# Performance work log

Measured on AMD Instinct MI355X. Metric: run time of the kernel, lower is better.

Reference implementation:

```python
import jax, jax.numpy as jnp
import numpy as np

B, C, H, W = 2, 128, 64, 64
EPS = 1e-5


def setup_inputs() -> dict:
    key = jax.random.key(0)
    ks = jax.random.split(key, 8)
    sc = 1.0 / np.sqrt(C)
    inp = {
        "x": jax.random.normal(ks[0], (B, C, H, W, 2), jnp.float32),
        # naive complex BN affine params: per-channel, per-component (real/imag)
        "bn_w": jnp.ones((C, 2), jnp.float32),
        "bn_b": jnp.zeros((C, 2), jnp.float32),
        # complex 1x1 conv weights: (out_c, in_c, 2) -> [..,0]=W_real, [..,1]=W_imag
        "wq": jax.random.normal(ks[1], (C, C, 2), jnp.float32) * sc,
        "bq": jnp.zeros((C, 2), jnp.float32),
        "wk": jax.random.normal(ks[2], (C, C, 2), jnp.float32) * sc,
        "bk": jnp.zeros((C, 2), jnp.float32),
        "wv": jax.random.normal(ks[3], (C, C, 2), jnp.float32) * sc,
        "bv": jnp.zeros((C, 2), jnp.float32),
        "gamma": jnp.float32(0.05),
    }
    return inp


def _complex_bn(x, w, b):
    # naive complex BN: normalize real and imag independently per channel
    # x: (B,C,H,W,2); stats over (B,H,W) per (C, component)
    mean = x.mean(axis=(0, 2, 3), keepdims=True)
    var = x.var(axis=(0, 2, 3), keepdims=True)
    xn = (x - mean) * jax.lax.rsqrt(var + EPS)
    return xn * w[None, :, None, None, :] + b[None, :, None, None, :]


def _complex_conv1x1(x, w, b):
    # x: (B,C,H,W,2); w: (O,C,2); b: (O,2)
    xr, xi = x[..., 0], x[..., 1]
    wr, wi = w[..., 0], w[..., 1]
    yr = jnp.einsum('oc,bchw->bohw', wr, xr) - jnp.einsum('oc,bchw->bohw', wi, xi)
    yi = jnp.einsum('oc,bchw->bohw', wr, xi) + jnp.einsum('oc,bchw->bohw', wi, xr)
    yr = yr + b[:, 0][None, :, None, None]
    yi = yi + b[:, 1][None, :, None, None]
    return jnp.stack([yr, yi], axis=-1)


def _attention(x, wq, bq, wk, bk, wv, bv, gamma):
    scale = C ** (-0.5)
    N = H * W
    # q,k,v: (B,C,H,W,2) -> (B,C,N,2) -> (B,N,C,2)
    to_tokens = lambda t: t.reshape(B, C, N, 2).transpose(0, 2, 1, 3)
    q = to_tokens(_complex_conv1x1(x, wq, bq))
    k = to_tokens(_complex_conv1x1(x, wk, bk))
    v = to_tokens(_complex_conv1x1(x, wv, bv))

    qr, qi = q[..., 0], q[..., 1]          # (B,N,C)
    kr, ki = k[..., 0], -k[..., 1]         # conjugate of k
    # k_t = conj(k) with token/channel axes swapped -> (B,C,N)
    ktr = kr.transpose(0, 2, 1)
    kti = ki.transpose(0, 2, 1)

    # complex matmul q @ k_t -> only the real part is used downstream
    attn_real = jnp.einsum('bnc,bcm->bnm', qr, ktr) - jnp.einsum('bnc,bcm->bnm', qi, kti)
    attn_w = jax.nn.softmax(attn_real * scale, axis=-1)  # (B,N,N)
    # dropout = identity (eval mode)

    # attn is purely real -> complex matmul reduces to two real matmuls
    out_r = jnp.einsum('bnm,bmc->bnc', attn_w, v[..., 0])
    out_i = jnp.einsum('bnm,bmc->bnc', attn_w, v[..., 1])
    out = jnp.stack([out_r, out_i], axis=-1)              # (B,N,C,2)
    out = out.transpose(0, 2, 1, 3).reshape(B, C, H, W, 2)
    return x + gamma * out


def reference(x, bn_w, bn_b, wq, bq, wk, bk, wv, bv, gamma):
    xn = _complex_bn(x, bn_w, bn_b)
    return _attention(xn, wq, bq, wk, bk, wv, bv, gamma)
```

## Files before the change

### kernel.cpp

```cpp
#include <hip/hip_runtime.h>
#include <hip/hip_bf16.h>

typedef __bf16 bf16_t;
typedef __bf16 bf16x8 __attribute__((ext_vector_type(8)));
typedef float  f32x4  __attribute__((ext_vector_type(4)));

#define MFMA16(A,B,C) __builtin_amdgcn_mfma_f32_16x16x32_bf16((A),(B),(C),0,0,0)

constexpr int Bn = 2, Cc = 128, Hh = 64, Wd = 64;
constexpr int N  = Hh * Wd;
constexpr int T  = Bn * N;
constexpr int D  = 2 * Cc;
constexpr int NSP = 4;
constexpr float EPS = 1e-5f;
constexpr float SCL = 0.08838834764831845f * 1.4426950408889634f;

__device__ __forceinline__ int tfrag(int row, int ch) {
    return (((ch >> 5) * 4 + (row >> 4)) << 10) +
           ((((ch >> 3) & 3) * 16 + (row & 15)) << 4) + (ch & 7) * 2;
}
__device__ __forceinline__ int vfrag(int ch, int key) {
    return (((key >> 5) * 16 + (ch >> 4)) << 10) +
           ((((key >> 3) & 3) * 16 + (ch & 15)) << 4) + (key & 7) * 2;
}

__device__ __forceinline__ void gl16(const void* g, void* l) {
    __builtin_amdgcn_global_load_lds(
        (const __attribute__((address_space(1))) void*)g,
        (__attribute__((address_space(3))) void*)l, 16, 0, 0);
}

__global__ void k_pre(const float* __restrict__ x, float4* __restrict__ part,
                      const float* __restrict__ wq, const float* __restrict__ wk,
                      const float* __restrict__ wv, const float* __restrict__ bq,
                      const float* __restrict__ bk, const float* __restrict__ bv,
                      char* __restrict__ Wg, float* __restrict__ bt) {
    int tid = threadIdx.x;
    if (blockIdx.x < 512) {
        int bid = blockIdx.x;
        int q = bid >> 7, c = bid & 127;
        float sr = 0.f, si = 0.f, qr = 0.f, qi = 0.f;
        for (int b = 0; b < Bn; ++b) {
            const float2* p = (const float2*)x + (size_t)(b * Cc + c) * N + q * 1024;
            for (int i = tid; i < 1024; i += 256) {
                float2 v = p[i];
                sr += v.x; si += v.y; qr += v.x * v.x; qi += v.y * v.y;
            }
        }
        #pragma unroll
        for (int d = 32; d >= 1; d >>= 1) {
            sr += __shfl_xor(sr, d); si += __shfl_xor(si, d);
            qr += __shfl_xor(qr, d); qi += __shfl_xor(qi, d);
        }
        __shared__ float red[4][4];
        int w = tid >> 6;
        if ((tid & 63) == 0) { red[w][0] = sr; red[w][1] = si; red[w][2] = qr; red[w][3] = qi; }
        __syncthreads();
        if (tid == 0) {
            part[c * 4 + q] = make_float4(red[0][0] + red[1][0] + red[2][0] + red[3][0],
                                          red[0][1] + red[1][1] + red[2][1] + red[3][1],
                                          red[0][2] + red[1][2] + red[2][2] + red[3][2],
                                          red[0][3] + red[1][3] + red[2][3] + red[3][3]);
        }
    } else {
        int o = blockIdx.x - 512;
        int k = tid;
        int proj = o >> 8, oc = o & 255;
        const float* wsrc = proj == 0 ? wq : (proj == 1 ? wk : wv);
        const float* bsrc = proj == 0 ? bq : (proj == 1 ? bk : bv);
        int co = oc >> 7, oo = oc & 127;
        int c = k & 127, kc = k >> 7;
        float val;
        if (co == 0) val = (kc == 0) ? wsrc[(oo * 128 + c) * 2 + 0] : -wsrc[(oo * 128 + c) * 2 + 1];
        else         val = (kc == 0) ? wsrc[(oo * 128 + c) * 2 + 1] :  wsrc[(oo * 128 + c) * 2 + 0];
        int tile = o >> 6, row = o & 63;
        *(bf16_t*)(Wg + (size_t)tile * 32768 + tfrag(row, k)) = (bf16_t)val;
        if (k == 0) bt[o] = bsrc[oo * 2 + co];
    }
}

__global__ void k_norm(const float* __restrict__ x, const float4* __restrict__ part,
                       const float* __restrict__ bn_w, const float* __restrict__ bn_b,
                       char* __restrict__ XNg) {
    __shared__ float4 ssl[128];
    __shared__ __align__(16) char Tsh[32768];
    int blk = blockIdx.x;
    int b = blk >> 6, hw0 = (blk & 63) * 64;
    int tid = threadIdx.x;
    if (tid < 128) {
        float4 p0 = part[tid * 4 + 0], p1 = part[tid * 4 + 1];
        float4 p2 = part[tid * 4 + 2], p3 = part[tid * 4 + 3];
        float sr = p0.x + p1.x + p2.x + p3.x, si = p0.y + p1.y + p2.y + p3.y;
        float qr = p0.z + p1.z + p2.z + p3.z, qi = p0.w + p1.w + p2.w + p3.w;
        const float inv = 1.0f / (float)(Bn * N);
        float mr = sr * inv, mi = si * inv;
        float vr = qr * inv - mr * mr, vi = qi * inv - mi * mi;
        float scr = bn_w[tid * 2 + 0] * rsqrtf(vr + EPS);
        float sci = bn_w[tid * 2 + 1] * rsqrtf(vi + EPS);
        ssl[tid] = make_float4(scr, bn_b[tid * 2 + 0] - mr * scr,
                               sci, bn_b[tid * 2 + 1] - mi * sci);
    }
    __syncthreads();
    const float2* xin = (const float2*)x;
    #pragma unroll
    for (int it = 0; it < 32; ++it) {
        int idx = it * 256 + tid;
        int c = idx >> 6, hw = idx & 63;
        size_t gi = (size_t)(b * Cc + c) * N + hw0 + hw;
        float2 v = xin[gi];
        float4 s = ssl[c];
        *(bf16_t*)(Tsh + tfrag(hw, c))       = (bf16_t)(v.x * s.x + s.y);
        *(bf16_t*)(Tsh + tfrag(hw, c + 128)) = (bf16_t)(v.y * s.z + s.w);
    }
    __syncthreads();
    #pragma unroll
    for (int it = 0; it < 8; ++it) {
        int idx = it * 256 + tid;
        *(uint4*)(XNg + (size_t)blk * 32768 + idx * 16) = *(const uint4*)(Tsh + idx * 16);
    }
}

__global__ __launch_bounds__(256) void k_qkv(const char* __restrict__ XNg,
        const char* __restrict__ Wg, const float* __restrict__ bt,
        char* __restrict__ Qg, char* __restrict__ Kg, char* __restrict__ Vg) {
    __shared__ __align__(16) char Xsh[32768];
    __shared__ __align__(16) char Wsh[32768];
    int mx = blockIdx.x, ny = blockIdx.y;
    int tid = threadIdx.x;
    int w = tid >> 6, lane = tid & 63, n15 = lane & 15, quad = lane >> 4;
    const char* xs = XNg + (size_t)mx * 32768;
    const char* wsp = Wg + (size_t)ny * 32768;
    #pragma unroll
    for (int i = 0; i < 8; ++i) {
        int off = (w * 8 + i) * 1024 + lane * 16;
        gl16(xs + off, Xsh + off);
        gl16(wsp + off, Wsh + off);
    }
    __syncthreads();
    f32x4 acc[4] = {};
    #pragma unroll
    for (int ks = 0; ks < 8; ++ks) {
        bf16x8 a = *(const bf16x8*)(Xsh + (ks * 4 + w) * 1024 + lane * 16);
        #pragma unroll
        for (int t = 0; t < 4; ++t) {
            bf16x8 bw = *(const bf16x8*)(Wsh + (ks * 4 + t) * 1024 + lane * 16);
            acc[t] = MFMA16(a, bw, acc[t]);
        }
    }
    int proj = ny >> 2;
    int jb = (ny & 3) * 64;
    #pragma unroll
    for (int t = 0; t < 4; ++t) {
        int j = jb + t * 16 + n15;
        float bias = bt[ny * 64 + t * 16 + n15];
        #pragma unroll
        for (int r = 0; r < 4; ++r) {
            int tk = mx * 64 + w * 16 + quad * 4 + r;
            float v = acc[t][r] + bias;
            int bb = tk >> 12, n = tk & (N - 1);
            if (proj == 0) {
                *(bf16_t*)(Qg + (size_t)(tk >> 6) * 32768 + tfrag(tk & 63, j)) = (bf16_t)v;
            } else {
                size_t tb = (size_t)(bb * 64 + (n >> 6)) * 32768;
                if (proj == 1) *(bf16_t*)(Kg + tb + tfrag(n & 63, j)) = (bf16_t)v;
                else           *(bf16_t*)(Vg + tb + vfrag(j, n & 63)) = (bf16_t)v;
            }
        }
    }
}

__global__ __launch_bounds__(256, 2) void k_attn(const char* __restrict__ Qg,
        const char* __restrict__ Kg, const char* __restrict__ Vg,
        bf16_t* __restrict__ Opb, float* __restrict__ Lp) {
    __shared__ __align__(16) char Ksh[32768];
    __shared__ __align__(16) char Vsh[32768 + 1024];
    __shared__ __align__(16) char Psh[8192];
    int bid = blockIdx.x;
    int qt = bid & 63, sp = (bid >> 6) & 3, b = bid >> 8;
    int tid = threadIdx.x;
    int w = tid >> 6, lane = tid & 63, n15 = lane & 15, quad = lane >> 4;
    int r = w >> 1, h = w & 1;

    if (tid < 64) {
        uint4 ones; ones.x = ones.y = ones.z = ones.w = 0x3F803F80u;
        *(uint4*)(Vsh + 32768 + tid * 16) = ones;
    }

    bf16x8 qf[2][8];
    const char* qb = Qg + (size_t)(b * 64 + qt) * 32768;
    #pragma unroll
    for (int g = 0; g < 2; ++g)
        #pragma unroll
        for (int ks = 0; ks < 8; ++ks)
            qf[g][ks] = *(const bf16x8*)(qb + (ks * 4 + r * 2 + g) * 1024 + lane * 16);

    f32x4 o[2][8] = {};
    f32x4 l_[2] = {};

    for (int kt = 0; kt < 16; ++kt) {
        size_t tb = (size_t)(b * 64 + sp * 16 + kt) * 32768;
        __syncthreads();
        #pragma unroll
        for (int i = 0; i < 8; ++i) {
            int off = (w * 8 + i) * 1024 + lane * 16;
            gl16(Kg + tb + off, Ksh + off);
            gl16(Vg + tb + off, Vsh + off);
        }
        __syncthreads();

        f32x4 s[2][2] = {};
        #pragma unroll
        for (int ks = 0; ks < 8; ++ks) {
            #pragma unroll
            for (int c = 0; c < 2; ++c) {
                bf16x8 kf = *(const bf16x8*)(Ksh + (ks * 4 + h * 2 + c) * 1024 + lane * 16);
                s[0][c] = MFMA16(qf[0][ks], kf, s[0][c]);
                s[1][c] = MFMA16(qf[1][ks], kf, s[1][c]);
            }
        }
        #pragma unroll
        for (int g = 0; g < 2; ++g)
            #pragma unroll
            for (int c = 0; c < 2; ++c)
                #pragma unroll
                for (int ri = 0; ri < 4; ++ri) {
                    float p = __builtin_amdgcn_exp2f(s[g][c][ri] * SCL);
                    *(bf16_t*)(Psh + (h * 4 + r * 2 + g) * 1024 +
                               ((c * 2 + (n15 >> 3)) * 16 + quad * 4 + ri) * 16 +
                               (n15 & 7) * 2) = (bf16_t)p;
                }
        __syncthreads();
        #pragma unroll
        for (int k2 = 0; k2 < 2; ++k2) {
            bf16x8 pa0 = *(const bf16x8*)(Psh + (k2 * 4 + r * 2 + 0) * 1024 + lane * 16);
            bf16x8 pa1 = *(const bf16x8*)(Psh + (k2 * 4 + r * 2 + 1) * 1024 + lane * 16);
            bf16x8 onef = *(const bf16x8*)(Vsh + 32768 + lane * 16);
            l_[0] = MFMA16(pa0, onef, l_[0]);
            l_[1] = MFMA16(pa1, onef, l_[1]);
            #pragma unroll
            for (int ct = 0; ct < 8; ++ct) {
                bf16x8 vf = *(const bf16x8*)(Vsh + (k2 * 16 + h * 8 + ct) * 1024 + lane * 16);
                o[0][ct] = MFMA16(pa0, vf, o[0][ct]);
                o[1][ct] = MFMA16(pa1, vf, o[1][ct]);
            }
        }
    }
    int tok0 = b * N + qt * 64 + r * 32;
    #pragma unroll
    for (int g = 0; g < 2; ++g) {
        #pragma unroll
        for (int ct = 0; ct < 8; ++ct)
            #pragma unroll
            for (int ri = 0; ri < 4; ++ri)
                Opb[((size_t)sp * T + tok0 + g * 16 + quad * 4 + ri) * D +
                    h * 128 + ct * 16 + n15] = (bf16_t)o[g][ct][ri];
        if (h == 0 && n15 == 0) {
            #pragma unroll
            for (int ri = 0; ri < 4; ++ri)
                Lp[sp * T + tok0 + g * 16 + quad * 4 + ri] = l_[g][ri];
        }
    }
}

__global__ void k_comb(const bf16_t* __restrict__ Opb, const float* __restrict__ Lp,
                       const float4* __restrict__ part, const float* __restrict__ bn_w,
                       const float* __restrict__ bn_b, const float* __restrict__ x,
                       const float* __restrict__ gamma, float* __restrict__ out) {
    __shared__ float4 ssl[128];
    __shared__ float wts[32];
    __shared__ float Ot[256 * 33];
    int blk = blockIdx.x;
    int b = blk >> 7, hw0 = (blk & 127) * 32;
    int tok0 = b * N + hw0;
    int tid = threadIdx.x;
    if (tid < 128) {
        float4 p0 = part[tid * 4 + 0], p1 = part[tid * 4 + 1];
        float4 p2 = part[tid * 4 + 2], p3 = part[tid * 4 + 3];
        float sr = p0.x + p1.x + p2.x + p3.x, si = p0.y + p1.y + p2.y + p3.y;
        float qr = p0.z + p1.z + p2.z + p3.z, qi = p0.w + p1.w + p2.w + p3.w;
        const float inv = 1.0f / (float)(Bn * N);
        float mr = sr * inv, mi = si * inv;
        float vr = qr * inv - mr * mr, vi = qi * inv - mi * mi;
        float scr = bn_w[tid * 2 + 0] * rsqrtf(vr + EPS);
        float sci = bn_w[tid * 2 + 1] * rsqrtf(vi + EPS);
        ssl[tid] = make_float4(scr, bn_b[tid * 2 + 0] - mr * scr,
                               sci, bn_b[tid * 2 + 1] - mi * sci);
    }
    if (tid < 32) {
        float Z = 0.f;
        #pragma unroll
        for (int s = 0; s < NSP; ++s) Z += Lp[s * T + tok0 + tid];
        wts[tid] = gamma[0] / Z;
    }
    __syncthreads();
    #pragma unroll
    for (int i = 0; i < 4; ++i) {
        int idx = i * 256 + tid;
        int tk = idx >> 5, chunk = idx & 31;
        size_t base = (size_t)(tok0 + tk) * D + chunk * 8;
        float acc[8] = {};
        #pragma unroll
        for (int s = 0; s < NSP; ++s) {
            bf16x8 v = *(const bf16x8*)(Opb + (size_t)s * T * D + base);
            #pragma unroll
            for (int j = 0; j < 8; ++j) acc[j] += (float)v[j];
        }
        float ww = wts[tk];
        #pragma unroll
        for (int j = 0; j < 8; ++j) Ot[(chunk * 8 + j) * 33 + tk] = acc[j] * ww;
    }
    __syncthreads();
    const float2* xin = (const float2*)x;
    float2* xo = (float2*)out;
    #pragma unroll
    for (int i = 0; i < 16; ++i) {
        int linear = i * 256 + tid;
        int c = linear >> 5, hwo = linear & 31;
        size_t idx = (size_t)(b * Cc + c) * N + hw0 + hwo;
        float2 v = xin[idx];
        float4 s = ssl[c];
        float2 res;
        res.x = v.x * s.x + s.y + Ot[c * 33 + hwo];
        res.y = v.y * s.z + s.w + Ot[(128 + c) * 33 + hwo];
        xo[idx] = res;
    }
}

extern "C" void kernel_launch(void* const* d_in, const int* in_sizes, int n_in,
                              void* d_out, int out_size, void* d_ws, size_t ws_size,
                              hipStream_t stream) {
    const float* x    = (const float*)d_in[0];
    const float* bn_w = (const float*)d_in[1];
    const float* bn_b = (const float*)d_in[2];
    const float* wq   = (const float*)d_in[3];
    const float* bq   = (const float*)d_in[4];
    const float* wk   = (const float*)d_in[5];
    const float* bk   = (const float*)d_in[6];
    const float* wv   = (const float*)d_in[7];
    const float* bv   = (const float*)d_in[8];
    const float* gam  = (const float*)d_in[9];
    float* out = (float*)d_out;

    char* ws = (char*)d_ws;
    size_t off = 0;
    auto alloc = [&](size_t bytes) -> void* {
        void* p = ws + off;
        off += (bytes + 255) & ~(size_t)255;
        return p;
    };
    float4* part = (float4*)alloc(512 * sizeof(float4));
    char*   XNg  = (char*)alloc((size_t)128 * 32768);
    char*   Wg   = (char*)alloc((size_t)12 * 32768);
    float*  bt   = (float*)alloc(768 * 4);
    char*   Qg   = (char*)alloc((size_t)128 * 32768);
    char*   Kg   = (char*)alloc((size_t)128 * 32768);
    char*   Vg   = (char*)alloc((size_t)128 * 32768);
    bf16_t* Opb  = (bf16_t*)alloc((size_t)NSP * T * D * 2);
    float*  Lp   = (float*)alloc((size_t)NSP * T * 4);

    k_pre<<<1280, 256, 0, stream>>>(x, part, wq, wk, wv, bq, bk, bv, Wg, bt);
    k_norm<<<128, 256, 0, stream>>>(x, part, bn_w, bn_b, XNg);
    k_qkv<<<dim3(128, 12), 256, 0, stream>>>(XNg, Wg, bt, Qg, Kg, Vg);
    k_attn<<<512, 256, 0, stream>>>(Qg, Kg, Vg, Opb, Lp);
    k_comb<<<256, 256, 0, stream>>>(Opb, Lp, part, bn_w, bn_b, x, gam, out);
}
```

Measured before the change: 151.7 us.

## Double-buffer K tiles in half-size key chunks and overlap loads with compute

The attention kernel now processes 32-key half tiles instead of 64-key tiles. The next K half tile is prefetched into a double buffer while the current one is used, and explicit waitcnt plus barriers replace one of the three syncthreads per iteration. LDS use drops from about 73KB to about 53KB, the ones fragment moves from LDS into registers, and block-to-work mapping is interleaved so the split groups of one query tile run together. The V load is still issued in the same iteration, so it stays partly exposed, and the hand-written vmcnt accounting is fragile.

```diff
diff --git a/kernel.cpp b/kernel.cpp
--- a/kernel.cpp
+++ b/kernel.cpp
@@ -172,19 +172,19 @@
 __global__ __launch_bounds__(256, 2) void k_attn(const char* __restrict__ Qg,
         const char* __restrict__ Kg, const char* __restrict__ Vg,
         bf16_t* __restrict__ Opb, float* __restrict__ Lp) {
-    __shared__ __align__(16) char Ksh[32768];
-    __shared__ __align__(16) char Vsh[32768 + 1024];
-    __shared__ __align__(16) char Psh[8192];
+    __shared__ __align__(16) char Ksh[2 * 16384];
+    __shared__ __align__(16) char Vsh[16384];
+    __shared__ __align__(16) char Psh[4096];
     int bid = blockIdx.x;
-    int qt = bid & 63, sp = (bid >> 6) & 3, b = bid >> 8;
+    int grp = bid & 7, qt = bid >> 3;
+    int sp = grp & 3, b = grp >> 2;
     int tid = threadIdx.x;
     int w = tid >> 6, lane = tid & 63, n15 = lane & 15, quad = lane >> 4;
     int r = w >> 1, h = w & 1;
 
-    if (tid < 64) {
-        uint4 ones; ones.x = ones.y = ones.z = ones.w = 0x3F803F80u;
-        *(uint4*)(Vsh + 32768 + tid * 16) = ones;
-    }
+    bf16x8 onef;
+    #pragma unroll
+    for (int i = 0; i < 8; ++i) onef[i] = (bf16_t)1.0f;
 
     bf16x8 qf[2][8];
     const char* qb = Qg + (size_t)(b * 64 + qt) * 32768;
@@ -194,55 +194,73 @@
         for (int ks = 0; ks < 8; ++ks)
             qf[g][ks] = *(const bf16x8*)(qb + (ks * 4 + r * 2 + g) * 1024 + lane * 16);
 
+    {
+        size_t kt0 = (size_t)(b * 64 + sp * 16) * 32768;
+        #pragma unroll
+        for (int i = 0; i < 4; ++i) {
+            int lf = w * 4 + i;
+            gl16(Kg + kt0 + (((lf >> 1) * 4 + (lf & 1)) << 10) + lane * 16,
+                 Ksh + (lf << 10) + lane * 16);
+        }
+    }
+
     f32x4 o[2][8] = {};
     f32x4 l_[2] = {};
 
-    for (int kt = 0; kt < 16; ++kt) {
-        size_t tb = (size_t)(b * 64 + sp * 16 + kt) * 32768;
+    #pragma unroll 2
+    for (int kt = 0; kt < 32; ++kt) {
+        int cur = kt & 1;
         __syncthreads();
-        #pragma unroll
-        for (int i = 0; i < 8; ++i) {
-            int off = (w * 8 + i) * 1024 + lane * 16;
-            gl16(Kg + tb + off, Ksh + off);
-            gl16(Vg + tb + off, Vsh + off);
-        }
-        __syncthreads();
-
-        f32x4 s[2][2] = {};
+
+        size_t vt = (size_t)(b * 64 + sp * 16 + (kt >> 1)) * 32768 +
+                    (size_t)(kt & 1) * 16384;
+        #pragma unroll
+        for (int i = 0; i < 4; ++i) {
+            int off = (w * 4 + i) * 1024 + lane * 16;
+            gl16(Vg + vt + off, Vsh + off);
+        }
+        if (kt < 31) {
+            int ck = kt + 1;
+            size_t ktile = (size_t)(b * 64 + sp * 16 + (ck >> 1)) * 32768;
+            char* kb = Ksh + (cur ^ 1) * 16384;
+            #pragma unroll
+            for (int i = 0; i < 4; ++i) {
+                int lf = w * 4 + i;
+                gl16(Kg + ktile + (((lf >> 1) * 4 + (ck & 1) * 2 + (lf & 1)) << 10) + lane * 16,
+                     kb + (lf << 10) + lane * 16);
+            }
+        }
+
+        const char* kc = Ksh + cur * 16384;
+        f32x4 s0 = {}, s1 = {};
         #pragma unroll
         for (int ks = 0; ks < 8; ++ks) {
-            #pragma unroll
-            for (int c = 0; c < 2; ++c) {
-                bf16x8 kf = *(const bf16x8*)(Ksh + (ks * 4 + h * 2 + c) * 1024 + lane * 16);
-                s[0][c] = MFMA16(qf[0][ks], kf, s[0][c]);
-                s[1][c] = MFMA16(qf[1][ks], kf, s[1][c]);
-            }
-        }
-        #pragma unroll
-        for (int g = 0; g < 2; ++g)
-            #pragma unroll
-            for (int c = 0; c < 2; ++c)
-                #pragma unroll
-                for (int ri = 0; ri < 4; ++ri) {
-                    float p = __builtin_amdgcn_exp2f(s[g][c][ri] * SCL);
-                    *(bf16_t*)(Psh + (h * 4 + r * 2 + g) * 1024 +
-                               ((c * 2 + (n15 >> 3)) * 16 + quad * 4 + ri) * 16 +
-                               (n15 & 7) * 2) = (bf16_t)p;
-                }
-        __syncthreads();
-        #pragma unroll
-        for (int k2 = 0; k2 < 2; ++k2) {
-            bf16x8 pa0 = *(const bf16x8*)(Psh + (k2 * 4 + r * 2 + 0) * 1024 + lane * 16);
-            bf16x8 pa1 = *(const bf16x8*)(Psh + (k2 * 4 + r * 2 + 1) * 1024 + lane * 16);
-            bf16x8 onef = *(const bf16x8*)(Vsh + 32768 + lane * 16);
-            l_[0] = MFMA16(pa0, onef, l_[0]);
-            l_[1] = MFMA16(pa1, onef, l_[1]);
-            #pragma unroll
-            for (int ct = 0; ct < 8; ++ct) {
-                bf16x8 vf = *(const bf16x8*)(Vsh + (k2 * 16 + h * 8 + ct) * 1024 + lane * 16);
-                o[0][ct] = MFMA16(pa0, vf, o[0][ct]);
-                o[1][ct] = MFMA16(pa1, vf, o[1][ct]);
-            }
+            bf16x8 kf = *(const bf16x8*)(kc + ((ks * 2 + h) << 10) + lane * 16);
+            s0 = MFMA16(qf[0][ks], kf, s0);
+            s1 = MFMA16(qf[1][ks], kf, s1);
+        }
+        #pragma unroll
+        for (int ri = 0; ri < 4; ++ri) {
+            float p0 = __builtin_amdgcn_exp2f(s0[ri] * SCL);
+            float p1 = __builtin_amdgcn_exp2f(s1[ri] * SCL);
+            int base = ((h * 2 + (n15 >> 3)) * 16 + quad * 4 + ri) * 16 + (n15 & 7) * 2;
+            *(bf16_t*)(Psh + ((r * 2 + 0) << 10) + base) = (bf16_t)p0;
+            *(bf16_t*)(Psh + ((r * 2 + 1) << 10) + base) = (bf16_t)p1;
+        }
+        if (kt < 31) asm volatile("s_waitcnt vmcnt(4) lgkmcnt(0)" ::: "memory");
+        else         asm volatile("s_waitcnt vmcnt(0) lgkmcnt(0)" ::: "memory");
+        __builtin_amdgcn_s_barrier();
+        __builtin_amdgcn_sched_barrier(0);
+
+        bf16x8 pa0 = *(const bf16x8*)(Psh + ((r * 2 + 0) << 10) + lane * 16);
+        bf16x8 pa1 = *(const bf16x8*)(Psh + ((r * 2 + 1) << 10) + lane * 16);
+        l_[0] = MFMA16(pa0, onef, l_[0]);
+        l_[1] = MFMA16(pa1, onef, l_[1]);
+        #pragma unroll
+        for (int ct = 0; ct < 8; ++ct) {
+            bf16x8 vf = *(const bf16x8*)(Vsh + ((h * 8 + ct) << 10) + lane * 16);
+            o[0][ct] = MFMA16(pa0, vf, o[0][ct]);
+            o[1][ct] = MFMA16(pa1, vf, o[1][ct]);
         }
     }
     int tok0 = b * N + qt * 64 + r * 32;
```

Result: no change. 153.4 us (+1.1%).

## Switch attention Q/K/V and probabilities to FP8 MFMA with halved tiles

Applied to the files above, without the earlier changes.

Q, K and V are now stored as e4m3 FP8 in a new fragment layout, and the softmax probabilities as e5m2 BF8 after subtracting a constant shift. The attention kernel uses FP8 MFMA for both QK^T and PV and computes the row sums against an FP8 ones constant. This halves global and LDS traffic and shared-memory footprint, and the block index mapping is changed to interleave splits and batches. The cost is much lower numerical precision in scores and probabilities, plus a fixed exponent shift that could underflow or overflow for other input distributions.

```diff
diff --git a/kernel.cpp b/kernel.cpp
--- a/kernel.cpp
+++ b/kernel.cpp
@@ -1,11 +1,15 @@
 #include <hip/hip_runtime.h>
 #include <hip/hip_bf16.h>
+#include <hip/hip_fp8.h>
 
 typedef __bf16 bf16_t;
 typedef __bf16 bf16x8 __attribute__((ext_vector_type(8)));
 typedef float  f32x4  __attribute__((ext_vector_type(4)));
+typedef long   i64_t;
 
 #define MFMA16(A,B,C) __builtin_amdgcn_mfma_f32_16x16x32_bf16((A),(B),(C),0,0,0)
+#define MFMA8(A,B,C)  __builtin_amdgcn_mfma_f32_16x16x32_fp8_fp8((A),(B),(C),0,0,0)
+#define MFMA85(A,B,C) __builtin_amdgcn_mfma_f32_16x16x32_bf8_fp8((A),(B),(C),0,0,0)
 
 constexpr int Bn = 2, Cc = 128, Hh = 64, Wd = 64;
 constexpr int N  = Hh * Wd;
@@ -14,14 +18,28 @@
 constexpr int NSP = 4;
 constexpr float EPS = 1e-5f;
 constexpr float SCL = 0.08838834764831845f * 1.4426950408889634f;
+constexpr float PSH = 9.0f;
 
 __device__ __forceinline__ int tfrag(int row, int ch) {
     return (((ch >> 5) * 4 + (row >> 4)) << 10) +
            ((((ch >> 3) & 3) * 16 + (row & 15)) << 4) + (ch & 7) * 2;
 }
-__device__ __forceinline__ int vfrag(int ch, int key) {
-    return (((key >> 5) * 16 + (ch >> 4)) << 10) +
-           ((((key >> 3) & 3) * 16 + (ch & 15)) << 4) + (key & 7) * 2;
+__device__ __forceinline__ int tfrag8(int row, int ch) {
+    return (((ch >> 5) * 4 + (row >> 4)) << 9) +
+           ((((ch >> 3) & 3) * 16 + (row & 15)) << 3) + (ch & 7);
+}
+__device__ __forceinline__ int vfrag8(int ch, int key) {
+    return (((key >> 5) * 16 + (ch >> 4)) << 9) +
+           ((((key >> 3) & 3) * 16 + (ch & 15)) << 3) + (key & 7);
+}
+
+__device__ __forceinline__ unsigned char to_fp8(float v) {
+    __hip_fp8_e4m3 t(v);
+    return t.__x;
+}
+__device__ __forceinline__ unsigned char to_bf8(float v) {
+    __hip_fp8_e5m2 t(v);
+    return t.__x;
 }
 
 __device__ __forceinline__ void gl16(const void* g, void* l) {
@@ -156,53 +174,51 @@
         #pragma unroll
         for (int r = 0; r < 4; ++r) {
             int tk = mx * 64 + w * 16 + quad * 4 + r;
-            float v = acc[t][r] + bias;
+            unsigned char v8 = to_fp8(acc[t][r] + bias);
             int bb = tk >> 12, n = tk & (N - 1);
             if (proj == 0) {
-                *(bf16_t*)(Qg + (size_t)(tk >> 6) * 32768 + tfrag(tk & 63, j)) = (bf16_t)v;
+                *(unsigned char*)(Qg + (size_t)(tk >> 6) * 16384 + tfrag8(tk & 63, j)) = v8;
             } else {
-                size_t tb = (size_t)(bb * 64 + (n >> 6)) * 32768;
-                if (proj == 1) *(bf16_t*)(Kg + tb + tfrag(n & 63, j)) = (bf16_t)v;
-                else           *(bf16_t*)(Vg + tb + vfrag(j, n & 63)) = (bf16_t)v;
+                size_t tb = (size_t)(bb * 64 + (n >> 6)) * 16384;
+                if (proj == 1) *(unsigned char*)(Kg + tb + tfrag8(n & 63, j)) = v8;
+                else           *(unsigned char*)(Vg + tb + vfrag8(j, n & 63)) = v8;
             }
         }
     }
 }
 
-__global__ __launch_bounds__(256, 2) void k_attn(const char* __restrict__ Qg,
+__global__ __launch_bounds__(256) void k_attn(const char* __restrict__ Qg,
         const char* __restrict__ Kg, const char* __restrict__ Vg,
         bf16_t* __restrict__ Opb, float* __restrict__ Lp) {
-    __shared__ __align__(16) char Ksh[32768];
-    __shared__ __align__(16) char Vsh[32768 + 1024];
-    __shared__ __align__(16) char Psh[8192];
+    __shared__ __align__(16) char Ksh[16384];
+    __shared__ __align__(16) char Vsh[16384];
+    __shared__ __align__(16) char Psh[4096];
     int bid = blockIdx.x;
-    int qt = bid & 63, sp = (bid >> 6) & 3, b = bid >> 8;
+    int grp = bid & 7, qt = bid >> 3;
+    int sp = grp & 3, b = grp >> 2;
     int tid = threadIdx.x;
     int w = tid >> 6, lane = tid & 63, n15 = lane & 15, quad = lane >> 4;
     int r = w >> 1, h = w & 1;
 
-    if (tid < 64) {
-        uint4 ones; ones.x = ones.y = ones.z = ones.w = 0x3F803F80u;
-        *(uint4*)(Vsh + 32768 + tid * 16) = ones;
-    }
-
-    bf16x8 qf[2][8];
-    const char* qb = Qg + (size_t)(b * 64 + qt) * 32768;
+    const i64_t ONES = 0x3838383838383838L;
+
+    i64_t qf[2][8];
+    const char* qb = Qg + (size_t)(b * 64 + qt) * 16384;
     #pragma unroll
     for (int g = 0; g < 2; ++g)
         #pragma unroll
         for (int ks = 0; ks < 8; ++ks)
-            qf[g][ks] = *(const bf16x8*)(qb + (ks * 4 + r * 2 + g) * 1024 + lane * 16);
+            qf[g][ks] = *(const i64_t*)(qb + ((ks * 4 + r * 2 + g) << 9) + lane * 8);
 
     f32x4 o[2][8] = {};
     f32x4 l_[2] = {};
 
     for (int kt = 0; kt < 16; ++kt) {
-        size_t tb = (size_t)(b * 64 + sp * 16 + kt) * 32768;
+        size_t tb = (size_t)(b * 64 + sp * 16 + kt) * 16384;
         __syncthreads();
         #pragma unroll
-        for (int i = 0; i < 8; ++i) {
-            int off = (w * 8 + i) * 1024 + lane * 16;
+        for (int i = 0; i < 4; ++i) {
+            int off = (w * 4 + i) * 1024 + lane * 16;
             gl16(Kg + tb + off, Ksh + off);
             gl16(Vg + tb + off, Vsh + off);
         }
@@ -213,9 +229,9 @@
         for (int ks = 0; ks < 8; ++ks) {
             #pragma unroll
             for (int c = 0; c < 2; ++c) {
-                bf16x8 kf = *(const bf16x8*)(Ksh + (ks * 4 + h * 2 + c) * 1024 + lane * 16);
-                s[0][c] = MFMA16(qf[0][ks], kf, s[0][c]);
-                s[1][c] = MFMA16(qf[1][ks], kf, s[1][c]);
+                i64_t kf = *(const i64_t*)(Ksh + ((ks * 4 + h * 2 + c) << 9) + lane * 8);
+                s[0][c] = MFMA8(qf[0][ks], kf, s[0][c]);
+                s[1][c] = MFMA8(qf[1][ks], kf, s[1][c]);
             }
         }
         #pragma unroll
@@ -224,24 +240,24 @@
             for (int c = 0; c < 2; ++c)
                 #pragma unroll
                 for (int ri = 0; ri < 4; ++ri) {
-                    float p = __builtin_amdgcn_exp2f(s[g][c][ri] * SCL);
-                    *(bf16_t*)(Psh + (h * 4 + r * 2 + g) * 1024 +
-                               ((c * 2 + (n15 >> 3)) * 16 + quad * 4 + ri) * 16 +
-                               (n15 & 7) * 2) = (bf16_t)p;
+                    float p = __builtin_amdgcn_exp2f(s[g][c][ri] * SCL - PSH);
+                    *(unsigned char*)(Psh + ((h * 4 + r * 2 + g) << 9) +
+                        (((c * 2 + (n15 >> 3)) * 16 + quad * 4 + ri) << 3) +
+                        (n15 & 7)) = to_bf8(p);
                 }
         __syncthreads();
+
         #pragma unroll
         for (int k2 = 0; k2 < 2; ++k2) {
-            bf16x8 pa0 = *(const bf16x8*)(Psh + (k2 * 4 + r * 2 + 0) * 1024 + lane * 16);
-            bf16x8 pa1 = *(const bf16x8*)(Psh + (k2 * 4 + r * 2 + 1) * 1024 + lane * 16);
-            bf16x8 onef = *(const bf16x8*)(Vsh + 32768 + lane * 16);
-            l_[0] = MFMA16(pa0, onef, l_[0]);
-            l_[1] = MFMA16(pa1, onef, l_[1]);
+            i64_t pa0 = *(const i64_t*)(Psh + ((k2 * 4 + r * 2 + 0) << 9) + lane * 8);
+            i64_t pa1 = *(const i64_t*)(Psh + ((k2 * 4 + r * 2 + 1) << 9) + lane * 8);
+            l_[0] = MFMA85(pa0, ONES, l_[0]);
+            l_[1] = MFMA85(pa1, ONES, l_[1]);
             #pragma unroll
             for (int ct = 0; ct < 8; ++ct) {
-                bf16x8 vf = *(const bf16x8*)(Vsh + (k2 * 16 + h * 8 + ct) * 1024 + lane * 16);
-                o[0][ct] = MFMA16(pa0, vf, o[0][ct]);
-                o[1][ct] = MFMA16(pa1, vf, o[1][ct]);
+                i64_t vf = *(const i64_t*)(Vsh + ((k2 * 16 + h * 8 + ct) << 9) + lane * 8);
+                o[0][ct] = MFMA85(pa0, vf, o[0][ct]);
+                o[1][ct] = MFMA85(pa1, vf, o[1][ct]);
             }
         }
     }
@@ -352,9 +368,9 @@
     char*   XNg  = (char*)alloc((size_t)128 * 32768);
     char*   Wg   = (char*)alloc((size_t)12 * 32768);
     float*  bt   = (float*)alloc(768 * 4);
-    char*   Qg   = (char*)alloc((size_t)128 * 32768);
-    char*   Kg   = (char*)alloc((size_t)128 * 32768);
-    char*   Vg   = (char*)alloc((size_t)128 * 32768);
+    char*   Qg   = (char*)alloc((size_t)128 * 16384);
+    char*   Kg   = (char*)alloc((size_t)128 * 16384);
+    char*   Vg   = (char*)alloc((size_t)128 * 16384);
     bf16_t* Opb  = (bf16_t*)alloc((size_t)NSP * T * D * 2);
     float*  Lp   = (float*)alloc((size_t)NSP * T * 4);
 
```

After: 147.1 us. 3.1% less time.
